# Performance work log

Hardware: AMD Instinct MI355X
Metric: run time of the kernel (lower is better)

The kernel has to match this reference:

```python
import jax, jax.numpy as jnp
import numpy as np

B, N = 16, 8192

# batched gather: pts [N,C], ind [S,K] -> [S,K,C]
_bgather = jax.vmap(lambda pts, ind: pts[ind])


def _fps(xyz, npoint):
    """Farthest point sampling. xyz [B,N,3] -> idx [B,npoint] int32."""
    b, n, _ = xyz.shape
    def step(carry, _):
        mind, last = carry
        p = jax.vmap(lambda pts, i: pts[i])(xyz, last)  # [B,3]
        d = jnp.sum((xyz - p[:, None, :]) ** 2, axis=-1)  # [B,N]
        mind = jnp.minimum(mind, d)
        nxt = jnp.argmax(mind, axis=-1).astype(jnp.int32)
        return (mind, nxt), last
    init = (jnp.full((b, n), 1e10, xyz.dtype), jnp.zeros((b,), jnp.int32))
    _, idx = jax.lax.scan(step, init, None, length=npoint)
    return jnp.transpose(idx)  # [B,npoint]


def _ball_query(xyz, new_xyz, radius, nsample):
    """xyz [B,N,3], new_xyz [B,S,3] -> idx [B,S,nsample] int32.
    First nsample points within radius; slots past the count filled with first hit
    (matches pointnet2 CUDA ball_query semantics)."""
    n = xyz.shape[1]
    # squared distances without materializing [B,S,N,3]
    d2 = (jnp.sum(new_xyz ** 2, -1)[:, :, None]
          + jnp.sum(xyz ** 2, -1)[:, None, :]
          - 2.0 * jnp.einsum('bsc,bnc->bsn', new_xyz, xyz))  # [B,S,N]
    key = jnp.where(d2 < radius * radius, jnp.arange(n, dtype=jnp.int32), n)
    idx = jnp.sort(key, axis=-1)[..., :nsample]  # first in-radius indices
    first = idx[..., :1]
    idx = jnp.where(idx == n, first, idx)  # pad with first hit
    return jnp.clip(idx, 0, n - 1)


def _mlp(g, layers):
    # g [B,S,K,C]; shared 1x1-conv MLP with folded BN, ReLU
    for W, b in layers:
        g = jax.nn.relu(jnp.einsum('bskc,oc->bsko', g, W) + b)
    return g


def _sa(xyz, feat, npoint, radius, nsample, layers):
    fidx = _fps(xyz, npoint)
    new_xyz = _bgather(xyz, fidx)  # [B,S,3]
    idx = _ball_query(xyz, new_xyz, radius, nsample)  # [B,S,K]
    g = _bgather(xyz, idx) - new_xyz[:, :, None, :]  # centered grouped xyz
    if feat is not None:
        g = jnp.concatenate([g, _bgather(feat, idx)], axis=-1)
    g = _mlp(g, layers)
    return new_xyz, jnp.max(g, axis=2)  # [B,S,Cout]


def setup_inputs() -> dict:
    key = jax.random.key(0)
    ks = jax.random.split(key, 13)
    def w(k, o, i):
        return (jax.random.normal(k, (o, i), jnp.float32) * 0.1)
    inp = {
        'x': jax.random.uniform(ks[0], (B, N, 3), jnp.float32),
        'W1a': w(ks[1], 64, 3),    'b1a': jnp.zeros((64,), jnp.float32),
        'W1b': w(ks[2], 128, 64),  'b1b': jnp.zeros((128,), jnp.float32),
        'W2a': w(ks[3], 128, 131), 'b2a': jnp.zeros((128,), jnp.float32),
        'W2b': w(ks[4], 256, 128), 'b2b': jnp.zeros((256,), jnp.float32),
        'W3a': w(ks[5], 512, 259), 'b3a': jnp.zeros((512,), jnp.float32),
        'W3b': w(ks[6], 1024, 512),'b3b': jnp.zeros((1024,), jnp.float32),
    }
    return inp


def reference(x, W1a, b1a, W1b, b1b, W2a, b2a, W2b, b2b, W3a, b3a, W3b, b3b):
    xyz = x[..., 0:3]  # input_feat_dim=0 -> no extra features
    # sa1: npoint=512, r=0.2, k=64, mlp 3->64->128 (use_xyz)
    xyz1, feat1 = _sa(xyz, None, 512, 0.2, 64, [(W1a, b1a), (W1b, b1b)])
    # sa2: npoint=128, r=0.4, k=64, mlp 131->128->256
    xyz2, feat2 = _sa(xyz1, feat1, 128, 0.4, 64, [(W2a, b2a), (W2b, b2b)])
    # sa3: group-all, mlp 259->512->1024
    g = jnp.concatenate([xyz2, feat2], axis=-1)[:, None]  # [B,1,128,259]
    g = _mlp(g, [(W3a, b3a), (W3b, b3b)])
    return jnp.max(g, axis=2)[:, 0]  # [B,1024]
```

## Files before the change

kernel.cpp:

```cpp
#include <hip/hip_runtime.h>

#define B 16
#define N 8192
#define S1 512
#define S2 128
#define K 64

template<int CTRL>
__device__ __forceinline__ float dpp_max_f32(float v) {
  unsigned o = (unsigned)__builtin_amdgcn_update_dpp(
      (int)__float_as_uint(v), (int)__float_as_uint(v), CTRL, 0xF, 0xF, false);
  return fmaxf(v, __uint_as_float(o));
}

__device__ __forceinline__ float wave_max_bcast(float v) {
  v = dpp_max_f32<0x111>(v);
  v = dpp_max_f32<0x112>(v);
  v = dpp_max_f32<0x114>(v);
  v = dpp_max_f32<0x118>(v);
  v = dpp_max_f32<0x142>(v);
  v = dpp_max_f32<0x143>(v);
  return __uint_as_float((unsigned)__builtin_amdgcn_readlane(
      (int)__float_as_uint(v), 63));
}

template<int NT, int PT, int MAXP, int MAXN>
__device__ __forceinline__ void fps_body(
    const float* __restrict__ pts, float* __restrict__ out_xyz,
    float* __restrict__ out2, int out2_stride, int n, int npoint) {
  const int b = blockIdx.x;
  const int t = threadIdx.x;
  const int w = t >> 6;
  const float* base = pts + (size_t)b * n * 3;
  __shared__ unsigned long long cell[3][4];
  __shared__ float s_out[MAXP * 3];
  __shared__ float s_pts[MAXN * 3];
  if (t < 12) ((unsigned long long*)cell)[t] = 0ull;
  float px[PT], py[PT], pz[PT], mind[PT];
#pragma unroll
  for (int i = 0; i < PT; i++) {
    int p = t + i * NT;
    px[i] = base[p * 3 + 0];
    py[i] = base[p * 3 + 1];
    pz[i] = base[p * 3 + 2];
    mind[i] = 1e10f;
    s_pts[p * 3 + 0] = px[i];
    s_pts[p * 3 + 1] = py[i];
    s_pts[p * 3 + 2] = pz[i];
  }
  float cx = base[0], cy = base[1], cz = base[2];
  __syncthreads();
  for (int it = 0; it < npoint; it++) {
    if (t == 0) {
      s_out[it * 3 + 0] = cx; s_out[it * 3 + 1] = cy; s_out[it * 3 + 2] = cz;
    }
    float bv = -1.0f;
#pragma unroll
    for (int i = 0; i < PT; i++) {
      float dx = px[i] - cx, dy = py[i] - cy, dz = pz[i] - cz;
      float d = dx * dx;
      d = fmaf(dy, dy, d);
      d = fmaf(dz, dz, d);
      float md = fminf(mind[i], d);
      mind[i] = md;
      bv = fmaxf(bv, md);
    }
    float gm = wave_max_bcast(bv);
    if (bv == gm) {
      int bi = 0;
#pragma unroll
      for (int i = PT - 1; i >= 0; i--)
        if (mind[i] == bv) bi = i;
      unsigned long long kk = ((unsigned long long)__float_as_uint(bv) << 32) |
                              (~(unsigned)(t + bi * NT));
      atomicMax(&cell[it % 3][w & 3], kk);
    }
    if (t < 4) cell[(it + 1) % 3][t] = 0ull;
    __syncthreads();
    unsigned long long k0 = cell[it % 3][0];
    unsigned long long k1 = cell[it % 3][1];
    unsigned long long k2 = cell[it % 3][2];
    unsigned long long k3 = cell[it % 3][3];
    unsigned long long wk = k0 > k1 ? k0 : k1;
    unsigned long long wk2 = k2 > k3 ? k2 : k3;
    if (wk2 > wk) wk = wk2;
    int ui = __builtin_amdgcn_readfirstlane((int)(~(unsigned)wk));
    const float* q = s_pts + ui * 3;
    cx = q[0]; cy = q[1]; cz = q[2];
  }
  for (int e = t; e < npoint * 3; e += NT)
    out_xyz[(size_t)b * npoint * 3 + e] = s_out[e];
  if (out2) {
    for (int e = t; e < npoint; e += NT) {
      float* o2 = out2 + ((size_t)b * npoint + e) * out2_stride;
      o2[0] = s_out[e * 3 + 0];
      o2[1] = s_out[e * 3 + 1];
      o2[2] = s_out[e * 3 + 2];
    }
  }
}

__global__ __launch_bounds__(1024) __attribute__((amdgpu_waves_per_eu(4, 4)))
void fps1_kernel(const float* __restrict__ pts, float* __restrict__ out_xyz,
                 float* __restrict__ out2, int out2_stride, int n, int npoint) {
  fps_body<1024, 8, 512, 8192>(pts, out_xyz, out2, out2_stride, n, npoint);
}

__global__ __launch_bounds__(512) __attribute__((amdgpu_waves_per_eu(2, 2)))
void fps2_kernel(const float* __restrict__ pts, float* __restrict__ out_xyz,
                 float* __restrict__ out2, int out2_stride, int n, int npoint) {
  fps_body<512, 1, 128, 512>(pts, out_xyz, out2, out2_stride, n, npoint);
}

__global__ __launch_bounds__(256) void ballq_kernel(
    const float* __restrict__ pts, const float* __restrict__ ctr,
    int* __restrict__ idx, int n, int ns, int total, float r2) {
  int gid = blockIdx.x * blockDim.x + threadIdx.x;
  int wid = gid >> 6;
  int lane = threadIdx.x & 63;
  if (wid >= total) return;
  int b = wid / ns, s = wid - b * ns;
  const float* pb = pts + (size_t)b * n * 3;
  const float* c = ctr + ((size_t)b * ns + s) * 3;
  float cx = c[0], cy = c[1], cz = c[2];
  float sc = cx * cx + cy * cy + cz * cz;
  int* out = idx + ((size_t)b * ns + s) * K;
  int cnt = 0, first = n - 1;
  for (int base = 0; base < n && cnt < K; base += 64) {
    int p = base + lane;
    float x = pb[p * 3 + 0], y = pb[p * 3 + 1], z = pb[p * 3 + 2];
    float sp = x * x + y * y + z * z;
    float dot = cx * x + cy * y + cz * z;
    float d2 = sc + sp - 2.0f * dot;
    bool inr = d2 < r2;
    unsigned long long m = __ballot(inr);
    if (cnt == 0 && m != 0ull) first = base + __ffsll((long long)m) - 1;
    int pre = (int)__popcll(m & ((1ull << lane) - 1ull));
    if (inr && (cnt + pre) < K) out[cnt + pre] = p;
    cnt += (int)__popcll(m);
  }
  if (cnt > K) cnt = K;
  if (lane >= cnt) out[lane] = first;
}

__global__ __launch_bounds__(256) void sa1_kernel(
    const float* __restrict__ xyz, const int* __restrict__ idx,
    const float* __restrict__ ctr, const float* __restrict__ W1a,
    const float* __restrict__ b1a, const float* __restrict__ W1b,
    const float* __restrict__ b1b, float* __restrict__ feat) {
  __shared__ float s_l[K][3];
  __shared__ float s_h[K][64];
  __shared__ float s_red[128];
  int blk = blockIdx.x;
  int b = blk >> 9, s = blk & 511;
  int tid = threadIdx.x;
  const int* gi = idx + ((size_t)b * S1 + s) * K;
  const float* c = ctr + ((size_t)b * S1 + s) * 3;
  float cx = c[0], cy = c[1], cz = c[2];
  if (tid < K) {
    int p = gi[tid];
    const float* q = xyz + ((size_t)b * N + p) * 3;
    s_l[tid][0] = q[0] - cx;
    s_l[tid][1] = q[1] - cy;
    s_l[tid][2] = q[2] - cz;
  }
  __syncthreads();
  for (int e = tid; e < K * 64; e += 256) {
    int k = e >> 6, o = e & 63;
    float v = b1a[o] + W1a[o * 3 + 0] * s_l[k][0] + W1a[o * 3 + 1] * s_l[k][1] +
              W1a[o * 3 + 2] * s_l[k][2];
    s_h[k][o] = fmaxf(v, 0.f);
  }
  __syncthreads();
  int o = tid & 127, half = tid >> 7;
  float w[64];
  const float4* wp = (const float4*)(W1b + o * 64);
#pragma unroll
  for (int c4 = 0; c4 < 16; c4++) {
    float4 t4 = wp[c4];
    w[c4 * 4 + 0] = t4.x; w[c4 * 4 + 1] = t4.y;
    w[c4 * 4 + 2] = t4.z; w[c4 * 4 + 3] = t4.w;
  }
  float bias = b1b[o];
  float m = -1e30f;
  int k0 = half * 32;
  for (int k = k0; k < k0 + 32; k++) {
    float acc = bias;
    const float4* hp = (const float4*)(&s_h[k][0]);
#pragma unroll
    for (int c4 = 0; c4 < 16; c4++) {
      float4 h = hp[c4];
      acc = fmaf(h.x, w[c4 * 4 + 0], acc);
      acc = fmaf(h.y, w[c4 * 4 + 1], acc);
      acc = fmaf(h.z, w[c4 * 4 + 2], acc);
      acc = fmaf(h.w, w[c4 * 4 + 3], acc);
    }
    m = fmaxf(m, acc);
  }
  if (half == 1) s_red[o] = m;
  __syncthreads();
  if (half == 0) {
    m = fmaxf(m, s_red[o]);
    feat[((size_t)b * S1 + s) * 128 + o] = fmaxf(m, 0.f);
  }
}

__global__ __launch_bounds__(256) void sa2_kernel(
    const float* __restrict__ xyz1, const float* __restrict__ feat1,
    const int* __restrict__ idx, const float* __restrict__ ctr,
    const float* __restrict__ W2a, const float* __restrict__ b2a,
    const float* __restrict__ W2b, const float* __restrict__ b2b,
    float* __restrict__ in3) {
  __shared__ int s_pi[K];
  __shared__ float s_g[K][132];
  __shared__ float s_h[K][128];
  __shared__ float s_red[256];
  int blk = blockIdx.x;
  int b = blk >> 7, s = blk & 127;
  int tid = threadIdx.x;
  const int* gi = idx + ((size_t)b * S2 + s) * K;
  const float* c = ctr + ((size_t)b * S2 + s) * 3;
  float cx = c[0], cy = c[1], cz = c[2];
  if (tid < K) {
    int p = gi[tid];
    s_pi[tid] = p;
    const float* q = xyz1 + ((size_t)b * S1 + p) * 3;
    s_g[tid][0] = q[0] - cx;
    s_g[tid][1] = q[1] - cy;
    s_g[tid][2] = q[2] - cz;
  }
  __syncthreads();
  for (int e = tid; e < K * 128; e += 256) {
    int k = e >> 7, f = e & 127;
    s_g[k][3 + f] = feat1[((size_t)b * S1 + s_pi[k]) * 128 + f];
  }
  __syncthreads();
  {
    int o = tid & 127, half = tid >> 7, k0 = half * 32;
    const float* wr = W2a + o * 131;
    float acc[32];
    float bias = b2a[o];
#pragma unroll
    for (int j = 0; j < 32; j++) acc[j] = bias;
    for (int c4 = 0; c4 < 32; c4++) {
      float w0 = wr[c4 * 4 + 0], w1 = wr[c4 * 4 + 1];
      float w2 = wr[c4 * 4 + 2], w3 = wr[c4 * 4 + 3];
#pragma unroll
      for (int j = 0; j < 32; j++) {
        float4 g = *(const float4*)(&s_g[k0 + j][c4 * 4]);
        acc[j] = fmaf(g.x, w0, acc[j]);
        acc[j] = fmaf(g.y, w1, acc[j]);
        acc[j] = fmaf(g.z, w2, acc[j]);
        acc[j] = fmaf(g.w, w3, acc[j]);
      }
    }
    float w0 = wr[128], w1 = wr[129], w2 = wr[130];
#pragma unroll
    for (int j = 0; j < 32; j++) {
      acc[j] = fmaf(s_g[k0 + j][128], w0, acc[j]);
      acc[j] = fmaf(s_g[k0 + j][129], w1, acc[j]);
      acc[j] = fmaf(s_g[k0 + j][130], w2, acc[j]);
      s_h[k0 + j][o] = fmaxf(acc[j], 0.f);
    }
  }
  __syncthreads();
  {
    int oa = tid & 127, half = tid >> 7, k0 = half * 32;
    const float4* wpa = (const float4*)(W2b + oa * 128);
    const float4* wpb = (const float4*)(W2b + (oa + 128) * 128);
    float acca[32], accb[32];
    float ba = b2b[oa], bb = b2b[oa + 128];
#pragma unroll
    for (int j = 0; j < 32; j++) { acca[j] = ba; accb[j] = bb; }
    for (int c4 = 0; c4 < 32; c4++) {
      float4 wa = wpa[c4];
      float4 wb = wpb[c4];
#pragma unroll
      for (int j = 0; j < 32; j++) {
        float4 h = *(const float4*)(&s_h[k0 + j][c4 * 4]);
        acca[j] = fmaf(h.x, wa.x, acca[j]);
        acca[j] = fmaf(h.y, wa.y, acca[j]);
        acca[j] = fmaf(h.z, wa.z, acca[j]);
        acca[j] = fmaf(h.w, wa.w, acca[j]);
        accb[j] = fmaf(h.x, wb.x, accb[j]);
        accb[j] = fmaf(h.y, wb.y, accb[j]);
        accb[j] = fmaf(h.z, wb.z, accb[j]);
        accb[j] = fmaf(h.w, wb.w, accb[j]);
      }
    }
    float ma = -1e30f, mb = -1e30f;
#pragma unroll
    for (int j = 0; j < 32; j++) { ma = fmaxf(ma, acca[j]); mb = fmaxf(mb, accb[j]); }
    if (half == 1) { s_red[oa] = ma; s_red[oa + 128] = mb; }
    __syncthreads();
    if (half == 0) {
      ma = fmaxf(ma, s_red[oa]);
      mb = fmaxf(mb, s_red[oa + 128]);
      float* o3 = &in3[((size_t)b * S2 + s) * 259 + 3];
      o3[oa] = fmaxf(ma, 0.f);
      o3[oa + 128] = fmaxf(mb, 0.f);
    }
  }
}

__global__ __launch_bounds__(256) void mlp3a_kernel(
    const float* __restrict__ in3, const float* __restrict__ W3a,
    const float* __restrict__ b3a, float* __restrict__ h3) {
  __shared__ float s_wt[64][65];
  __shared__ float s_a[64][64];
  int blk = blockIdx.x;
  int b = blk >> 4, r = blk & 15;
  int ot = r >> 1, sh = r & 1;
  int tid = threadIdx.x;
  int o = tid & 63, sq = tid >> 6;
  float acc[16];
  float bias = b3a[ot * 64 + o];
#pragma unroll
  for (int j = 0; j < 16; j++) acc[j] = bias;
  for (int ch = 0; ch < 5; ch++) {
    int cb = ch * 64;
    int len = (ch == 4) ? 3 : 64;
    for (int e = tid; e < 4096; e += 256) {
      int oo = e >> 6, cc = e & 63;
      if (cc < len) s_wt[cc][oo] = W3a[(size_t)(ot * 64 + oo) * 259 + cb + cc];
    }
    for (int e = tid; e < 4096; e += 256) {
      int ss = e >> 6, cc = e & 63;
      if (cc < len) s_a[ss][cc] = in3[((size_t)b * S2 + sh * 64 + ss) * 259 + cb + cc];
    }
    __syncthreads();
    for (int cc = 0; cc < len; cc++) {
      float wv = s_wt[cc][o];
#pragma unroll
      for (int j = 0; j < 16; j++)
        acc[j] = fmaf(wv, s_a[sq * 16 + j][cc], acc[j]);
    }
    __syncthreads();
  }
#pragma unroll
  for (int j = 0; j < 16; j++) {
    int s = sh * 64 + sq * 16 + j;
    h3[((size_t)b * S2 + s) * 512 + ot * 64 + o] = fmaxf(acc[j], 0.f);
  }
}

__global__ __launch_bounds__(256) void mlp3b_kernel(
    const float* __restrict__ h3, const float* __restrict__ W3b,
    const float* __restrict__ b3b, float* __restrict__ out) {
  __shared__ float s_wt[64][65];
  __shared__ float s_h[128][64];
  __shared__ float s_red[4][64];
  int blk = blockIdx.x;
  int b = blk >> 4, ot = blk & 15;
  int tid = threadIdx.x;
  int o = tid & 63, sq = tid >> 6;
  float acc[32];
  float bias = b3b[ot * 64 + o];
#pragma unroll
  for (int j = 0; j < 32; j++) acc[j] = bias;
  for (int ch = 0; ch < 8; ch++) {
    int cb = ch * 64;
    for (int e = tid; e < 4096; e += 256) {
      int oo = e >> 6, cc = e & 63;
      s_wt[cc][oo] = W3b[(size_t)(ot * 64 + oo) * 512 + cb + cc];
    }
    for (int e = tid; e < 8192; e += 256) {
      int ss = e >> 6, cc = e & 63;
      s_h[ss][cc] = h3[((size_t)b * S2 + ss) * 512 + cb + cc];
    }
    __syncthreads();
    for (int c4 = 0; c4 < 16; c4++) {
      float w0 = s_wt[c4 * 4 + 0][o];
      float w1 = s_wt[c4 * 4 + 1][o];
      float w2 = s_wt[c4 * 4 + 2][o];
      float w3 = s_wt[c4 * 4 + 3][o];
#pragma unroll
      for (int j = 0; j < 32; j++) {
        float4 h = *(const float4*)(&s_h[sq * 32 + j][c4 * 4]);
        acc[j] = fmaf(h.x, w0, acc[j]);
        acc[j] = fmaf(h.y, w1, acc[j]);
        acc[j] = fmaf(h.z, w2, acc[j]);
        acc[j] = fmaf(h.w, w3, acc[j]);
      }
    }
    __syncthreads();
  }
  float m = -1e30f;
#pragma unroll
  for (int j = 0; j < 32; j++) m = fmaxf(m, acc[j]);
  s_red[sq][o] = m;
  __syncthreads();
  if (sq == 0) {
    m = fmaxf(fmaxf(s_red[0][o], s_red[1][o]), fmaxf(s_red[2][o], s_red[3][o]));
    out[(size_t)b * 1024 + ot * 64 + o] = fmaxf(m, 0.f);
  }
}

extern "C" void kernel_launch(void* const* d_in, const int* in_sizes, int n_in,
                              void* d_out, int out_size, void* d_ws, size_t ws_size,
                              hipStream_t stream) {
  const float* x = (const float*)d_in[0];
  const float* W1a = (const float*)d_in[1];
  const float* b1a = (const float*)d_in[2];
  const float* W1b = (const float*)d_in[3];
  const float* b1b = (const float*)d_in[4];
  const float* W2a = (const float*)d_in[5];
  const float* b2a = (const float*)d_in[6];
  const float* W2b = (const float*)d_in[7];
  const float* b2b = (const float*)d_in[8];
  const float* W3a = (const float*)d_in[9];
  const float* b3a = (const float*)d_in[10];
  const float* W3b = (const float*)d_in[11];
  const float* b3b = (const float*)d_in[12];
  float* out = (float*)d_out;

  float* nx1 = (float*)d_ws;
  int* idx1 = (int*)(nx1 + 16 * 512 * 3);
  float* feat1 = (float*)(idx1 + 16 * 512 * 64);
  float* nx2 = feat1 + 16 * 512 * 128;
  int* idx2 = (int*)(nx2 + 16 * 128 * 3);
  float* in3 = (float*)(idx2 + 16 * 128 * 64);
  float* h3 = in3 + 16 * 128 * 259;

  fps1_kernel<<<B, 1024, 0, stream>>>(x, nx1, nullptr, 0, N, S1);
  ballq_kernel<<<(B * S1) / 4, 256, 0, stream>>>(x, nx1, idx1, N, S1, B * S1, 0.04f);
  sa1_kernel<<<B * S1, 256, 0, stream>>>(x, idx1, nx1, W1a, b1a, W1b, b1b, feat1);
  fps2_kernel<<<B, 512, 0, stream>>>(nx1, nx2, in3, 259, S1, S2);
  ballq_kernel<<<(B * S2) / 4, 256, 0, stream>>>(nx1, nx2, idx2, S1, S2, B * S2, 0.16f);
  sa2_kernel<<<B * S2, 256, 0, stream>>>(nx1, feat1, idx2, nx2, W2a, b2a, W2b, b2b, in3);
  mlp3a_kernel<<<256, 256, 0, stream>>>(in3, W3a, b3a, h3);
  mlp3b_kernel<<<256, 256, 0, stream>>>(h3, W3b, b3b, out);
}
```

Before: 1.344 ms.

## Run second-stage FPS with a single wavefront per batch

Replaces the 512-thread FPS kernel for the 512-point second stage with a one-wave (64-thread) kernel that keeps 8 points per lane in registers. The per-iteration argmax uses a DPP wave reduction plus an LDS atomicMax on a double-buffered cell, with no block-wide barriers. The aim is to cut the cross-wave synchronisation cost in each of the 128 serial iterations. In exchange each lane does more arithmetic per iteration and only 16 waves run on the whole GPU.

New measurement: 1.372 ms. 1.02x slower.

```diff
diff --git a/kernel.cpp b/kernel.cpp
--- a/kernel.cpp
+++ b/kernel.cpp
@@ -106,10 +106,72 @@
   fps_body<1024, 8, 512, 8192>(pts, out_xyz, out2, out2_stride, n, npoint);
 }
 
-__global__ __launch_bounds__(512) __attribute__((amdgpu_waves_per_eu(2, 2)))
-void fps2_kernel(const float* __restrict__ pts, float* __restrict__ out_xyz,
-                 float* __restrict__ out2, int out2_stride, int n, int npoint) {
-  fps_body<512, 1, 128, 512>(pts, out_xyz, out2, out2_stride, n, npoint);
+template<int PT, int MAXP, int MAXN>
+__global__ __launch_bounds__(64) __attribute__((amdgpu_waves_per_eu(1, 1)))
+void fps_wave_kernel(const float* __restrict__ pts, float* __restrict__ out_xyz,
+                     float* __restrict__ out2, int out2_stride, int n, int npoint) {
+  const int b = blockIdx.x;
+  const int t = threadIdx.x;
+  const float* base = pts + (size_t)b * n * 3;
+  __shared__ unsigned long long cell[2];
+  __shared__ float s_out[MAXP * 3];
+  __shared__ float s_pts[MAXN * 3];
+  if (t < 2) cell[t] = 0ull;
+  float px[PT], py[PT], pz[PT], mind[PT];
+#pragma unroll
+  for (int i = 0; i < PT; i++) {
+    int p = t + i * 64;
+    px[i] = base[p * 3 + 0];
+    py[i] = base[p * 3 + 1];
+    pz[i] = base[p * 3 + 2];
+    mind[i] = 1e10f;
+    s_pts[p * 3 + 0] = px[i];
+    s_pts[p * 3 + 1] = py[i];
+    s_pts[p * 3 + 2] = pz[i];
+  }
+  float cx = base[0], cy = base[1], cz = base[2];
+  for (int it = 0; it < npoint; it++) {
+    if (t == 0) {
+      s_out[it * 3 + 0] = cx; s_out[it * 3 + 1] = cy; s_out[it * 3 + 2] = cz;
+    }
+    float bv = -1.0f;
+#pragma unroll
+    for (int i = 0; i < PT; i++) {
+      float dx = px[i] - cx, dy = py[i] - cy, dz = pz[i] - cz;
+      float d = dx * dx;
+      d = fmaf(dy, dy, d);
+      d = fmaf(dz, dz, d);
+      float md = fminf(mind[i], d);
+      mind[i] = md;
+      bv = fmaxf(bv, md);
+    }
+    float gm = wave_max_bcast(bv);
+    if (bv == gm) {
+      int bi = 0;
+#pragma unroll
+      for (int i = PT - 1; i >= 0; i--)
+        if (mind[i] == bv) bi = i;
+      unsigned long long kk = ((unsigned long long)__float_as_uint(bv) << 32) |
+                              (~(unsigned)(t + bi * 64));
+      atomicMax(&cell[it & 1], kk);
+    }
+    __threadfence_block();
+    unsigned long long wk = cell[it & 1];
+    if (t == 0) cell[(it + 1) & 1] = 0ull;
+    int ui = __builtin_amdgcn_readfirstlane((int)(~(unsigned)wk));
+    const float* q = s_pts + ui * 3;
+    cx = q[0]; cy = q[1]; cz = q[2];
+  }
+  for (int e = t; e < npoint * 3; e += 64)
+    out_xyz[(size_t)b * npoint * 3 + e] = s_out[e];
+  if (out2) {
+    for (int e = t; e < npoint; e += 64) {
+      float* o2 = out2 + ((size_t)b * npoint + e) * out2_stride;
+      o2[0] = s_out[e * 3 + 0];
+      o2[1] = s_out[e * 3 + 1];
+      o2[2] = s_out[e * 3 + 2];
+    }
+  }
 }
 
 __global__ __launch_bounds__(256) void ballq_kernel(
@@ -425,7 +487,7 @@
   fps1_kernel<<<B, 1024, 0, stream>>>(x, nx1, nullptr, 0, N, S1);
   ballq_kernel<<<(B * S1) / 4, 256, 0, stream>>>(x, nx1, idx1, N, S1, B * S1, 0.04f);
   sa1_kernel<<<B * S1, 256, 0, stream>>>(x, idx1, nx1, W1a, b1a, W1b, b1b, feat1);
-  fps2_kernel<<<B, 512, 0, stream>>>(nx1, nx2, in3, 259, S1, S2);
+  fps_wave_kernel<8, 128, 512><<<B, 64, 0, stream>>>(nx1, nx2, in3, 259, S1, S2);
   ballq_kernel<<<(B * S2) / 4, 256, 0, stream>>>(nx1, nx2, idx2, S1, S2, B * S2, 0.16f);
   sa2_kernel<<<B * S2, 256, 0, stream>>>(nx1, feat1, idx2, nx2, W2a, b2a, W2b, b2b, in3);
   mlp3a_kernel<<<256, 256, 0, stream>>>(in3, W3a, b3a, h3);
```
